# Optimization experiments

Measured on AMD Instinct MI355X. Metric: run time of the kernel, lower is better.

Reference implementation:

```python
import jax, jax.numpy as jnp
import numpy as np

B, S, D, H = 4, 2048, 512, 8
DK = D // H


def setup_inputs() -> dict:
    key = jax.random.key(0)
    ks = jax.random.split(key, 8)
    std = 1.0 / np.sqrt(D)
    return {
        "query": jax.random.normal(ks[0], (B, S, D), jnp.float32),
        "key": jax.random.normal(ks[1], (B, S, D), jnp.float32),
        "value": jax.random.normal(ks[2], (B, S, D), jnp.float32),
        "Wq": jax.random.normal(ks[3], (D, D), jnp.float32) * std,
        "Wk": jax.random.normal(ks[4], (D, D), jnp.float32) * std,
        "Wv": jax.random.normal(ks[5], (D, D), jnp.float32) * std,
        "Wo": jax.random.normal(ks[6], (D, D), jnp.float32) * std,
        "bo": jnp.zeros((D,), jnp.float32),
    }


def reference(query, key, value, Wq, Wk, Wv, Wo, bo):
    # nn.Linear stores weight [out, in]; y = x @ W.T
    def split_heads(x):  # [B,S,D] -> [B,H,S,DK]
        return x.reshape(B, S, H, DK).transpose(0, 2, 1, 3)

    Q = split_heads(query @ Wq.T)
    K = split_heads(key @ Wk.T)
    V = split_heads(value @ Wv.T)
    scale = jnp.sqrt(jnp.asarray(DK, Q.dtype))
    scores = jnp.einsum("bhqd,bhkd->bhqk", Q, K) / scale  # [B,H,S,S]
    attn = jax.nn.softmax(scores, axis=-1)  # dropout=0 / eval mode
    ctx = jnp.einsum("bhqk,bhkd->bhqd", attn, V)
    ctx = ctx.transpose(0, 2, 1, 3).reshape(B, S, D)
    return ctx @ Wo.T + bo
```

## Files before the change

### kernel.cpp

```cpp
#include <hip/hip_runtime.h>
#include <hip/hip_bf16.h>
#include <stdint.h>

#define DEV __device__ __forceinline__

typedef __attribute__((ext_vector_type(8))) __bf16 bf16x8;
typedef __attribute__((ext_vector_type(4))) float f32x4;
typedef __attribute__((ext_vector_type(16))) float f32x16;
typedef __attribute__((ext_vector_type(4))) short short4v;
typedef __attribute__((ext_vector_type(8))) short short8v;
typedef __attribute__((ext_vector_type(4))) unsigned int uint4v;

constexpr int B_ = 4, S_ = 2048, D_ = 512, H_ = 8, DK_ = 64;
constexpr int M_ = B_ * S_;
constexpr int K_ = D_;

DEV unsigned short f2bf(float f) {
  unsigned int u = __builtin_bit_cast(unsigned int, f);
  unsigned int r = (u + 0x7fffu + ((u >> 16) & 1u)) >> 16;
  return (unsigned short)r;
}

DEV void gld16(const void* g, void* l) {
  __builtin_amdgcn_global_load_lds(
      (const __attribute__((address_space(1))) unsigned int*)g,
      (__attribute__((address_space(3))) unsigned int*)l, 16, 0, 0);
}

DEV f32x4 mfma16(bf16x8 a, bf16x8 b, f32x4 c) {
  return __builtin_amdgcn_mfma_f32_16x16x32_bf16(a, b, c, 0, 0, 0);
}
DEV f32x16 mfma32(bf16x8 a, bf16x8 b, f32x16 c) {
  return __builtin_amdgcn_mfma_f32_32x32x16_bf16(a, b, c, 0, 0, 0);
}

DEV short4v tr16(const void* p) {
  short4v d;
  asm volatile("ds_read_b64_tr_b16 %0, %1"
               : "=v"(d)
               : "v"((const __attribute__((address_space(3))) char*)p));
  return d;
}

DEV unsigned pkbf(float a, float b) {
  unsigned r;
  asm("v_cvt_pk_bf16_f32 %0, %1, %2" : "=v"(r) : "v"(a), "v"(b));
  return r;
}

DEV void pl32swap(unsigned& a, unsigned& b) {
  asm volatile("v_permlane32_swap_b32 %0, %1" : "+v"(a), "+v"(b));
}

__global__ __launch_bounds__(256) void convert_all(
    const float* __restrict__ q, const float* __restrict__ k, const float* __restrict__ v,
    const float* __restrict__ wq, const float* __restrict__ wk,
    const float* __restrict__ wv, const float* __restrict__ wo,
    unsigned short* __restrict__ xq, unsigned short* __restrict__ xk,
    unsigned short* __restrict__ xv, unsigned short* __restrict__ wqb,
    unsigned short* __restrict__ wkb, unsigned short* __restrict__ wvb,
    unsigned short* __restrict__ wob)
{
  constexpr int NX = M_ * D_;
  constexpr int NW = D_ * D_;
  constexpr int TOT = (3 * NX + 4 * NW) / 4;
  for (int u = blockIdx.x * blockDim.x + threadIdx.x; u < TOT;
       u += gridDim.x * blockDim.x) {
    int e = u * 4;
    const float* src; unsigned short* dst; int off;
    if (e < 3 * NX) {
      int t = e >> 22; off = e & (NX - 1);
      src = (t == 0) ? q : ((t == 1) ? k : v);
      dst = (t == 0) ? xq : ((t == 1) ? xk : xv);
    } else {
      int e2 = e - 3 * NX;
      int t = e2 >> 18; off = e2 & (NW - 1);
      src = (t == 0) ? wq : ((t == 1) ? wk : ((t == 2) ? wv : wo));
      dst = (t == 0) ? wqb : ((t == 1) ? wkb : ((t == 2) ? wvb : wob));
    }
    float4 f = *(const float4*)(src + off);
    short4v o;
    o.x = (short)f2bf(f.x); o.y = (short)f2bf(f.y);
    o.z = (short)f2bf(f.z); o.w = (short)f2bf(f.w);
    *(short4v*)(dst + off) = o;
  }
}

template <int MODE>
__global__ __launch_bounds__(256, 4) void gemm_bt(
    const unsigned short* __restrict__ A0, const unsigned short* __restrict__ A1,
    const unsigned short* __restrict__ A2,
    const unsigned short* __restrict__ W0, const unsigned short* __restrict__ W1,
    const unsigned short* __restrict__ W2,
    unsigned short* __restrict__ O0, unsigned short* __restrict__ O1,
    unsigned short* __restrict__ O2,
    float* __restrict__ outF, const float* __restrict__ bias)
{
  constexpr int BM = (MODE == 0) ? 128 : 64;
  constexpr int BN = 128, BK = 64, NKT = K_ / BK;
  constexpr int AFR = BM / 32;
  __shared__ unsigned short As[BM * BK];
  __shared__ unsigned short Bs[BN * BK];
  const int tid = threadIdx.x, lane = tid & 63, wave = tid >> 6;
  const int z = blockIdx.z;
  const unsigned short* A = (MODE == 1 || z == 0) ? A0 : (z == 1 ? A1 : A2);
  const unsigned short* W = (MODE == 1 || z == 0) ? W0 : (z == 1 ? W1 : W2);
  unsigned short* outH = (MODE == 1 || z == 0) ? O0 : (z == 1 ? O1 : O2);
  const int bn0 = blockIdx.x * BN, bm0 = blockIdx.y * BM;
  const int wr = (wave >> 1) * (BM / 2), wc = (wave & 1) * 64;
  const int frow = lane & 15, fk16 = (lane >> 4) * 16;

  const char* srcA[AFR];
  int dstA[AFR];
#pragma unroll
  for (int i = 0; i < AFR; ++i) {
    int o = (wave * AFR + i) * 1024;
    int ol = o + lane * 16;
    int row = ol >> 7, off = (ol ^ ((row & 7) << 4)) & 127;
    srcA[i] = (const char*)A + (size_t)(bm0 + row) * (K_ * 2) + off;
    dstA[i] = o;
  }
  const char* srcB[4];
  int dstB[4];
#pragma unroll
  for (int i = 0; i < 4; ++i) {
    int o = (wave * 4 + i) * 1024;
    int ol = o + lane * 16;
    int row = ol >> 7, off = (ol ^ ((row & 7) << 4)) & 127;
    srcB[i] = (const char*)W + (size_t)(bn0 + row) * (K_ * 2) + off;
    dstB[i] = o;
  }

  f32x4 acc[AFR][4];
#pragma unroll
  for (int i = 0; i < AFR; ++i)
#pragma unroll
    for (int j = 0; j < 4; ++j)
#pragma unroll
      for (int r = 0; r < 4; ++r) acc[i][j][r] = 0.f;

  for (int kt = 0; kt < NKT; ++kt) {
    __syncthreads();
#pragma unroll
    for (int i = 0; i < AFR; ++i) gld16(srcA[i] + kt * 128, (char*)As + dstA[i]);
#pragma unroll
    for (int i = 0; i < 4; ++i)   gld16(srcB[i] + kt * 128, (char*)Bs + dstB[i]);
    __syncthreads();
#pragma unroll
    for (int kc = 0; kc < 2; ++kc) {
      bf16x8 a[AFR], b[4];
#pragma unroll
      for (int i = 0; i < AFR; ++i) {
        int row = wr + i * 16 + frow;
        a[i] = *(const bf16x8*)((const char*)As +
                ((row * 128 + kc * 64 + fk16) ^ ((row & 7) << 4)));
      }
#pragma unroll
      for (int j = 0; j < 4; ++j) {
        int row = wc + j * 16 + frow;
        b[j] = *(const bf16x8*)((const char*)Bs +
                ((row * 128 + kc * 64 + fk16) ^ ((row & 7) << 4)));
      }
      __builtin_amdgcn_s_setprio(1);
#pragma unroll
      for (int i = 0; i < AFR; ++i)
#pragma unroll
        for (int j = 0; j < 4; ++j)
          acc[i][j] = mfma16(a[i], b[j], acc[i][j]);
      __builtin_amdgcn_s_setprio(0);
    }
  }

  const int r0 = (lane >> 4) * 4, cn = lane & 15;
  float bv[4];
  if (MODE == 1) {
#pragma unroll
    for (int j = 0; j < 4; ++j) bv[j] = bias[bn0 + wc + j * 16 + cn];
  }
#pragma unroll
  for (int i = 0; i < AFR; ++i)
#pragma unroll
    for (int j = 0; j < 4; ++j)
#pragma unroll
      for (int r = 0; r < 4; ++r) {
        int gm = bm0 + wr + i * 16 + r0 + r;
        int gn = bn0 + wc + j * 16 + cn;
        float val = acc[i][j][r];
        if (MODE == 0) outH[(size_t)gm * D_ + gn] = f2bf(val);
        else           outF[(size_t)gm * D_ + gn] = val + bv[j];
      }
}

__global__ __launch_bounds__(256, 2) void attn(
    const unsigned short* __restrict__ Qm, const unsigned short* __restrict__ Km,
    const unsigned short* __restrict__ Vm, unsigned short* __restrict__ Ctx)
{
  constexpr int QB = 128, KVB = 64, NT = S_ / KVB;
  __shared__ unsigned short Qs[QB * DK_];
  __shared__ unsigned short Kd[2][KVB * DK_];
  __shared__ unsigned short Vd[2][KVB * DK_];
  __shared__ float smA[4][32];
  const int tid = threadIdx.x, lane = tid & 63, wave = tid >> 6;
  const int hi = lane >> 5, l31 = lane & 31, g1 = (lane >> 4) & 1;
  const int bh = blockIdx.y, q0 = blockIdx.x * QB;
  const int bq = bh >> 3, hh = bh & 7;
  const char* Qg = (const char*)(Qm + ((size_t)bq * S_ + q0) * D_ + hh * DK_);
  const char* Kg = (const char*)(Km + (size_t)bq * S_ * D_ + hh * DK_);
  const char* Vg = (const char*)(Vm + (size_t)bq * S_ * D_ + hh * DK_);

  auto stageSwz = [&](const char* gbase, unsigned short* lds, int o) {
    int ol = o + lane * 16;
    int row = ol >> 7, off = (ol ^ ((row & 7) << 4)) & 127;
    gld16(gbase + (size_t)row * 1024 + off, (char*)lds + o);
  };
  auto stageVt = [&](const char* gbase, unsigned short* lds, int o) {
    int ol = o + lane * 16;
    int E0 = ol >> 1;
    int st = E0 >> 6, rr = (E0 >> 4) & 3, c0 = E0 & 15;
    int kk = (st >> 2) * 4 + rr, dd = (st & 3) * 16 + c0;
    gld16(gbase + (size_t)kk * 1024 + dd * 2, (char*)lds + o);
  };

#pragma unroll
  for (int i = 0; i < 4; ++i) stageSwz(Qg, Qs, (wave * 4 + i) * 1024);
#pragma unroll
  for (int i = 0; i < 2; ++i) stageSwz(Kg, Kd[0], (wave * 2 + i) * 1024);
#pragma unroll
  for (int i = 0; i < 2; ++i) stageVt(Vg, Vd[0], (wave * 2 + i) * 1024);
  __syncthreads();

  bf16x8 qf[4];
  {
    int row = wave * 32 + l31;
    int rb = row * 128, sw = (row & 7) << 4;
#pragma unroll
    for (int c = 0; c < 4; ++c)
      qf[c] = *(const bf16x8*)((const char*)Qs + ((rb + c * 32 + hi * 16) ^ sw));
  }

  f32x16 oacc[2];
#pragma unroll
  for (int dt = 0; dt < 2; ++dt)
#pragma unroll
    for (int r = 0; r < 16; ++r) oacc[dt][r] = 0.f;
  float m2 = -1e30f, lsum = 0.f;
  constexpr float SCL2 = 0.125f * 1.44269504089f;

  int cur = 0;
  for (int t = 0; t < NT; ++t) {
    if (t + 1 < NT) {
      const char* Kg1 = Kg + (size_t)(t + 1) * KVB * 1024;
      const char* Vg1 = Vg + (size_t)(t + 1) * KVB * 1024;
#pragma unroll
      for (int i = 0; i < 2; ++i) stageSwz(Kg1, Kd[cur ^ 1], (wave * 2 + i) * 1024);
#pragma unroll
      for (int i = 0; i < 2; ++i) stageVt(Vg1, Vd[cur ^ 1], (wave * 2 + i) * 1024);
    }

    f32x16 sacc[2];
#pragma unroll
    for (int k2 = 0; k2 < 2; ++k2)
#pragma unroll
      for (int r = 0; r < 16; ++r) sacc[k2][r] = 0.f;
    __builtin_amdgcn_s_setprio(1);
#pragma unroll
    for (int c = 0; c < 4; ++c) {
#pragma unroll
      for (int k2 = 0; k2 < 2; ++k2) {
        int row = k2 * 32 + l31;
        bf16x8 kf = *(const bf16x8*)((const char*)Kd[cur] +
                     ((row * 128 + c * 32 + hi * 16) ^ ((row & 7) << 4)));
        sacc[k2] = mfma32(kf, qf[c], sacc[k2]);
      }
    }
    __builtin_amdgcn_s_setprio(0);

    float mloc = sacc[0][0];
#pragma unroll
    for (int k2 = 0; k2 < 2; ++k2)
#pragma unroll
      for (int r = 0; r < 16; ++r) mloc = fmaxf(mloc, sacc[k2][r]);
    mloc = fmaxf(mloc, __shfl_xor(mloc, 32));
    float m2n = fmaxf(m2, mloc * SCL2);
    float alpha = __builtin_amdgcn_exp2f(m2 - m2n);
    m2 = m2n;
    float psum = 0.f;
#pragma unroll
    for (int k2 = 0; k2 < 2; ++k2)
#pragma unroll
      for (int r = 0; r < 16; ++r) {
        float p = __builtin_amdgcn_exp2f(fmaf(sacc[k2][r], SCL2, -m2n));
        sacc[k2][r] = p;
        psum += p;
      }
    psum += __shfl_xor(psum, 32);
    lsum = lsum * alpha + psum;

    if (lane < 32) smA[wave][lane] = alpha;
    f32x4 av[4];
#pragma unroll
    for (int s = 0; s < 4; ++s)
      av[s] = *(const f32x4*)&smA[wave][s * 8 + hi * 4];
#pragma unroll
    for (int dt = 0; dt < 2; ++dt)
#pragma unroll
      for (int r = 0; r < 16; ++r) oacc[dt][r] *= av[r >> 2][r & 3];

    short4v va[4][2][2];
#pragma unroll
    for (int c = 0; c < 4; ++c)
#pragma unroll
      for (int dt = 0; dt < 2; ++dt) {
        int st = 16 * c + 8 * hi + 2 * dt + g1;
        const char* ad = (const char*)Vd[cur] + st * 128 + (lane & 15) * 8;
        va[c][dt][0] = tr16(ad);
        va[c][dt][1] = tr16(ad + 512);
      }
    bf16x8 pfrag[4];
#pragma unroll
    for (int c = 0; c < 4; ++c) {
      const f32x16& P = sacc[c >> 1];
      const int b = (c & 1) * 8;
      unsigned d0 = pkbf(P[b + 0], P[b + 1]);
      unsigned d1 = pkbf(P[b + 2], P[b + 3]);
      unsigned d2 = pkbf(P[b + 4], P[b + 5]);
      unsigned d3 = pkbf(P[b + 6], P[b + 7]);
      pl32swap(d0, d2);
      pl32swap(d1, d3);
      uint4v pi = {d0, d1, d2, d3};
      pfrag[c] = __builtin_bit_cast(bf16x8, pi);
    }
    asm volatile("s_waitcnt lgkmcnt(0)" ::: "memory");
    __builtin_amdgcn_sched_barrier(0);
    __builtin_amdgcn_s_setprio(1);
#pragma unroll
    for (int c = 0; c < 4; ++c)
#pragma unroll
      for (int dt = 0; dt < 2; ++dt) {
        short8v vv = __builtin_shufflevector(va[c][dt][0], va[c][dt][1],
                                             0, 1, 2, 3, 4, 5, 6, 7);
        oacc[dt] = mfma32(pfrag[c], __builtin_bit_cast(bf16x8, vv), oacc[dt]);
      }
    __builtin_amdgcn_s_setprio(0);

    __syncthreads();
    cur ^= 1;
  }

  if (lane < 32) smA[wave][lane] = 1.f / lsum;
  f32x4 iv[4];
#pragma unroll
  for (int s = 0; s < 4; ++s)
    iv[s] = *(const f32x4*)&smA[wave][s * 8 + hi * 4];
#pragma unroll
  for (int dt = 0; dt < 2; ++dt)
#pragma unroll
    for (int r = 0; r < 16; ++r) {
      int qq = (r & 3) + 8 * (r >> 2) + 4 * hi;
      int grow = q0 + wave * 32 + qq;
      int col = hh * 64 + dt * 32 + l31;
      Ctx[((size_t)bq * S_ + grow) * D_ + col] = f2bf(oacc[dt][r] * iv[r >> 2][r & 3]);
    }
}

extern "C" void kernel_launch(void* const* d_in, const int* in_sizes, int n_in,
                              void* d_out, int out_size, void* d_ws, size_t ws_size,
                              hipStream_t stream) {
  const float* q  = (const float*)d_in[0];
  const float* k  = (const float*)d_in[1];
  const float* v  = (const float*)d_in[2];
  const float* wq = (const float*)d_in[3];
  const float* wk = (const float*)d_in[4];
  const float* wv = (const float*)d_in[5];
  const float* wo = (const float*)d_in[6];
  const float* bo = (const float*)d_in[7];
  float* out = (float*)d_out;

  constexpr size_t NX = (size_t)M_ * D_;
  constexpr size_t NW = (size_t)D_ * D_;
  char* ws = (char*)d_ws;
  unsigned short* Xq  = (unsigned short*)ws; ws += NX * 2;
  unsigned short* Xk  = (unsigned short*)ws; ws += NX * 2;
  unsigned short* Xv  = (unsigned short*)ws; ws += NX * 2;
  unsigned short* Wqb = (unsigned short*)ws; ws += NW * 2;
  unsigned short* Wkb = (unsigned short*)ws; ws += NW * 2;
  unsigned short* Wvb = (unsigned short*)ws; ws += NW * 2;
  unsigned short* Wob = (unsigned short*)ws; ws += NW * 2;
  unsigned short* Qbf = (unsigned short*)ws; ws += NX * 2;
  unsigned short* Kbf = (unsigned short*)ws; ws += NX * 2;
  unsigned short* Vbf = (unsigned short*)ws; ws += NX * 2;
  unsigned short* Cx  = (unsigned short*)ws; ws += NX * 2;

  convert_all<<<2048, 256, 0, stream>>>(q, k, v, wq, wk, wv, wo,
                                        Xq, Xk, Xv, Wqb, Wkb, Wvb, Wob);
  gemm_bt<0><<<dim3(4, 64, 3), 256, 0, stream>>>(
      Xq, Xk, Xv, Wqb, Wkb, Wvb, Qbf, Kbf, Vbf, nullptr, nullptr);
  attn<<<dim3(S_ / 128, B_ * H_), 256, 0, stream>>>(Qbf, Kbf, Vbf, Cx);
  gemm_bt<1><<<dim3(4, 128, 1), 256, 0, stream>>>(
      Cx, nullptr, nullptr, Wob, nullptr, nullptr, nullptr, nullptr, nullptr,
      out, bo);
}
```

Measured before the change: 203.1 us.

## Fuse fp32 activation conversion into QKV GEMM and pipeline PV MFMA in attention

The QKV projection GEMM now reads fp32 activations directly and converts them to bf16 in registers before the LDS store, with register prefetch of the next K tile. This drops the separate conversion pass over the three large activation tensors and its round trip through workspace. In attention, the PV MFMA for tile t-1 is deferred into iteration t so it overlaps with the QK scores. The PV product is transposed (V as A operand) so the rescale alpha is per-lane, which removes the LDS broadcast of alpha and 1/lsum and allows packed 8-byte stores of the context. The risks are extra register pressure in both kernels and synchronous global loads for A in the QKV GEMM.

```diff
diff --git a/kernel.cpp b/kernel.cpp
--- a/kernel.cpp
+++ b/kernel.cpp
@@ -10,6 +10,7 @@
 typedef __attribute__((ext_vector_type(4))) short short4v;
 typedef __attribute__((ext_vector_type(8))) short short8v;
 typedef __attribute__((ext_vector_type(4))) unsigned int uint4v;
+typedef __attribute__((ext_vector_type(2))) unsigned int uint2v;
 
 constexpr int B_ = 4, S_ = 2048, D_ = 512, H_ = 8, DK_ = 64;
 constexpr int M_ = B_ * S_;
@@ -52,62 +53,141 @@
   asm volatile("v_permlane32_swap_b32 %0, %1" : "+v"(a), "+v"(b));
 }
 
-__global__ __launch_bounds__(256) void convert_all(
-    const float* __restrict__ q, const float* __restrict__ k, const float* __restrict__ v,
-    const float* __restrict__ wq, const float* __restrict__ wk,
-    const float* __restrict__ wv, const float* __restrict__ wo,
-    unsigned short* __restrict__ xq, unsigned short* __restrict__ xk,
-    unsigned short* __restrict__ xv, unsigned short* __restrict__ wqb,
-    unsigned short* __restrict__ wkb, unsigned short* __restrict__ wvb,
-    unsigned short* __restrict__ wob)
+__global__ __launch_bounds__(256) void convert_w(
+    const float* __restrict__ w0, const float* __restrict__ w1,
+    const float* __restrict__ w2, const float* __restrict__ w3,
+    unsigned short* __restrict__ o0, unsigned short* __restrict__ o1,
+    unsigned short* __restrict__ o2, unsigned short* __restrict__ o3)
 {
-  constexpr int NX = M_ * D_;
-  constexpr int NW = D_ * D_;
-  constexpr int TOT = (3 * NX + 4 * NW) / 4;
-  for (int u = blockIdx.x * blockDim.x + threadIdx.x; u < TOT;
-       u += gridDim.x * blockDim.x) {
-    int e = u * 4;
-    const float* src; unsigned short* dst; int off;
-    if (e < 3 * NX) {
-      int t = e >> 22; off = e & (NX - 1);
-      src = (t == 0) ? q : ((t == 1) ? k : v);
-      dst = (t == 0) ? xq : ((t == 1) ? xk : xv);
-    } else {
-      int e2 = e - 3 * NX;
-      int t = e2 >> 18; off = e2 & (NW - 1);
-      src = (t == 0) ? wq : ((t == 1) ? wk : ((t == 2) ? wv : wo));
-      dst = (t == 0) ? wqb : ((t == 1) ? wkb : ((t == 2) ? wvb : wob));
-    }
-    float4 f = *(const float4*)(src + off);
-    short4v o;
-    o.x = (short)f2bf(f.x); o.y = (short)f2bf(f.y);
-    o.z = (short)f2bf(f.z); o.w = (short)f2bf(f.w);
-    *(short4v*)(dst + off) = o;
-  }
-}
-
-template <int MODE>
-__global__ __launch_bounds__(256, 4) void gemm_bt(
-    const unsigned short* __restrict__ A0, const unsigned short* __restrict__ A1,
-    const unsigned short* __restrict__ A2,
+  int u = blockIdx.x * 256 + threadIdx.x;
+  int t = u >> 16, off = (u & 65535) * 4;
+  const float* src = (t == 0) ? w0 : (t == 1) ? w1 : (t == 2) ? w2 : w3;
+  unsigned short* dst = (t == 0) ? o0 : (t == 1) ? o1 : (t == 2) ? o2 : o3;
+  float4 f = *(const float4*)(src + off);
+  short4v o;
+  o.x = (short)f2bf(f.x); o.y = (short)f2bf(f.y);
+  o.z = (short)f2bf(f.z); o.w = (short)f2bf(f.w);
+  *(short4v*)(dst + off) = o;
+}
+
+__global__ __launch_bounds__(256, 3) void gemm_qkv(
+    const float* __restrict__ A0, const float* __restrict__ A1,
+    const float* __restrict__ A2,
     const unsigned short* __restrict__ W0, const unsigned short* __restrict__ W1,
     const unsigned short* __restrict__ W2,
     unsigned short* __restrict__ O0, unsigned short* __restrict__ O1,
-    unsigned short* __restrict__ O2,
-    float* __restrict__ outF, const float* __restrict__ bias)
+    unsigned short* __restrict__ O2)
 {
-  constexpr int BM = (MODE == 0) ? 128 : 64;
-  constexpr int BN = 128, BK = 64, NKT = K_ / BK;
-  constexpr int AFR = BM / 32;
+  constexpr int BM = 128, BN = 128, BK = 64, NKT = K_ / BK;
   __shared__ unsigned short As[BM * BK];
   __shared__ unsigned short Bs[BN * BK];
   const int tid = threadIdx.x, lane = tid & 63, wave = tid >> 6;
   const int z = blockIdx.z;
-  const unsigned short* A = (MODE == 1 || z == 0) ? A0 : (z == 1 ? A1 : A2);
-  const unsigned short* W = (MODE == 1 || z == 0) ? W0 : (z == 1 ? W1 : W2);
-  unsigned short* outH = (MODE == 1 || z == 0) ? O0 : (z == 1 ? O1 : O2);
+  const float* A = (z == 0) ? A0 : (z == 1 ? A1 : A2);
+  const unsigned short* W = (z == 0) ? W0 : (z == 1 ? W1 : W2);
+  unsigned short* outH = (z == 0) ? O0 : (z == 1 ? O1 : O2);
   const int bn0 = blockIdx.x * BN, bm0 = blockIdx.y * BM;
-  const int wr = (wave >> 1) * (BM / 2), wc = (wave & 1) * 64;
+  const int wr = (wave >> 1) * 64, wc = (wave & 1) * 64;
+  const int frow = lane & 15, fk16 = (lane >> 4) * 16;
+
+  const int srow = tid >> 1, scol = (tid & 1) * 32;
+  const float* asrc = A + (size_t)(bm0 + srow) * K_ + scol;
+  const int abase = srow * 128 + scol * 2, asw = (srow & 7) << 4;
+
+  const char* srcB[4];
+  int dstB[4];
+#pragma unroll
+  for (int i = 0; i < 4; ++i) {
+    int o = (wave * 4 + i) * 1024;
+    int ol = o + lane * 16;
+    int row = ol >> 7, off = (ol ^ ((row & 7) << 4)) & 127;
+    srcB[i] = (const char*)W + (size_t)(bn0 + row) * (K_ * 2) + off;
+    dstB[i] = o;
+  }
+
+  f32x4 acc[4][4];
+#pragma unroll
+  for (int i = 0; i < 4; ++i)
+#pragma unroll
+    for (int j = 0; j < 4; ++j)
+#pragma unroll
+      for (int r = 0; r < 4; ++r) acc[i][j][r] = 0.f;
+
+  float4 xv[8];
+#pragma unroll
+  for (int j = 0; j < 8; ++j) xv[j] = *(const float4*)(asrc + j * 4);
+
+  for (int kt = 0; kt < NKT; ++kt) {
+    __syncthreads();
+    {
+      unsigned dw[16];
+#pragma unroll
+      for (int j = 0; j < 8; ++j) {
+        dw[2 * j]     = pkbf(xv[j].x, xv[j].y);
+        dw[2 * j + 1] = pkbf(xv[j].z, xv[j].w);
+      }
+#pragma unroll
+      for (int c = 0; c < 4; ++c) {
+        uint4v q = {dw[4 * c], dw[4 * c + 1], dw[4 * c + 2], dw[4 * c + 3]};
+        *(uint4v*)((char*)As + ((abase + c * 16) ^ asw)) = q;
+      }
+    }
+#pragma unroll
+    for (int i = 0; i < 4; ++i) gld16(srcB[i] + kt * 128, (char*)Bs + dstB[i]);
+    __syncthreads();
+    if (kt + 1 < NKT) {
+#pragma unroll
+      for (int j = 0; j < 8; ++j)
+        xv[j] = *(const float4*)(asrc + (kt + 1) * 64 + j * 4);
+    }
+#pragma unroll
+    for (int kc = 0; kc < 2; ++kc) {
+      bf16x8 a[4], b[4];
+#pragma unroll
+      for (int i = 0; i < 4; ++i) {
+        int row = wr + i * 16 + frow;
+        a[i] = *(const bf16x8*)((const char*)As +
+                ((row * 128 + kc * 64 + fk16) ^ ((row & 7) << 4)));
+      }
+#pragma unroll
+      for (int j = 0; j < 4; ++j) {
+        int row = wc + j * 16 + frow;
+        b[j] = *(const bf16x8*)((const char*)Bs +
+                ((row * 128 + kc * 64 + fk16) ^ ((row & 7) << 4)));
+      }
+      __builtin_amdgcn_s_setprio(1);
+#pragma unroll
+      for (int i = 0; i < 4; ++i)
+#pragma unroll
+        for (int j = 0; j < 4; ++j)
+          acc[i][j] = mfma16(a[i], b[j], acc[i][j]);
+      __builtin_amdgcn_s_setprio(0);
+    }
+  }
+
+  const int r0 = (lane >> 4) * 4, cn = lane & 15;
+#pragma unroll
+  for (int i = 0; i < 4; ++i)
+#pragma unroll
+    for (int j = 0; j < 4; ++j)
+#pragma unroll
+      for (int r = 0; r < 4; ++r) {
+        int gm = bm0 + wr + i * 16 + r0 + r;
+        int gn = bn0 + wc + j * 16 + cn;
+        outH[(size_t)gm * D_ + gn] = f2bf(acc[i][j][r]);
+      }
+}
+
+__global__ __launch_bounds__(256, 4) void gemm_out(
+    const unsigned short* __restrict__ A, const unsigned short* __restrict__ W,
+    float* __restrict__ outF, const float* __restrict__ bias)
+{
+  constexpr int BM = 64, BN = 128, BK = 64, NKT = K_ / BK, AFR = 2;
+  __shared__ unsigned short As[BM * BK];
+  __shared__ unsigned short Bs[BN * BK];
+  const int tid = threadIdx.x, lane = tid & 63, wave = tid >> 6;
+  const int bn0 = blockIdx.x * BN, bm0 = blockIdx.y * BM;
+  const int wr = (wave >> 1) * 32, wc = (wave & 1) * 64;
   const int frow = lane & 15, fk16 = (lane >> 4) * 16;
 
   const char* srcA[AFR];
@@ -173,10 +253,8 @@
 
   const int r0 = (lane >> 4) * 4, cn = lane & 15;
   float bv[4];
-  if (MODE == 1) {
-#pragma unroll
-    for (int j = 0; j < 4; ++j) bv[j] = bias[bn0 + wc + j * 16 + cn];
-  }
+#pragma unroll
+  for (int j = 0; j < 4; ++j) bv[j] = bias[bn0 + wc + j * 16 + cn];
 #pragma unroll
   for (int i = 0; i < AFR; ++i)
 #pragma unroll
@@ -185,9 +263,7 @@
       for (int r = 0; r < 4; ++r) {
         int gm = bm0 + wr + i * 16 + r0 + r;
         int gn = bn0 + wc + j * 16 + cn;
-        float val = acc[i][j][r];
-        if (MODE == 0) outH[(size_t)gm * D_ + gn] = f2bf(val);
-        else           outF[(size_t)gm * D_ + gn] = val + bv[j];
+        outF[(size_t)gm * D_ + gn] = acc[i][j][r] + bv[j];
       }
 }
 
@@ -199,7 +275,6 @@
   __shared__ unsigned short Qs[QB * DK_];
   __shared__ unsigned short Kd[2][KVB * DK_];
   __shared__ unsigned short Vd[2][KVB * DK_];
-  __shared__ float smA[4][32];
   const int tid = threadIdx.x, lane = tid & 63, wave = tid >> 6;
   const int hi = lane >> 5, l31 = lane & 31, g1 = (lane >> 4) & 1;
   const int bh = blockIdx.y, q0 = blockIdx.x * QB;
@@ -246,6 +321,19 @@
   float m2 = -1e30f, lsum = 0.f;
   constexpr float SCL2 = 0.125f * 1.44269504089f;
 
+  short4v va[4][2][2];
+  bf16x8 pfrag[4];
+#pragma unroll
+  for (int c = 0; c < 4; ++c) {
+#pragma unroll
+    for (int dt = 0; dt < 2; ++dt) {
+      va[c][dt][0] = short4v{0, 0, 0, 0};
+      va[c][dt][1] = short4v{0, 0, 0, 0};
+    }
+    uint4v zz = {0u, 0u, 0u, 0u};
+    pfrag[c] = __builtin_bit_cast(bf16x8, zz);
+  }
+
   int cur = 0;
   for (int t = 0; t < NT; ++t) {
     if (t + 1 < NT) {
@@ -273,6 +361,14 @@
         sacc[k2] = mfma32(kf, qf[c], sacc[k2]);
       }
     }
+#pragma unroll
+    for (int c = 0; c < 4; ++c)
+#pragma unroll
+      for (int dt = 0; dt < 2; ++dt) {
+        short8v vv = __builtin_shufflevector(va[c][dt][0], va[c][dt][1],
+                                             0, 1, 2, 3, 4, 5, 6, 7);
+        oacc[dt] = mfma32(__builtin_bit_cast(bf16x8, vv), pfrag[c], oacc[dt]);
+      }
     __builtin_amdgcn_s_setprio(0);
 
     float mloc = sacc[0][0];
@@ -296,17 +392,11 @@
     psum += __shfl_xor(psum, 32);
     lsum = lsum * alpha + psum;
 
-    if (lane < 32) smA[wave][lane] = alpha;
-    f32x4 av[4];
-#pragma unroll
-    for (int s = 0; s < 4; ++s)
-      av[s] = *(const f32x4*)&smA[wave][s * 8 + hi * 4];
 #pragma unroll
     for (int dt = 0; dt < 2; ++dt)
 #pragma unroll
-      for (int r = 0; r < 16; ++r) oacc[dt][r] *= av[r >> 2][r & 3];
-
-    short4v va[4][2][2];
+      for (int r = 0; r < 16; ++r) oacc[dt][r] *= alpha;
+
 #pragma unroll
     for (int c = 0; c < 4; ++c)
 #pragma unroll
@@ -316,7 +406,6 @@
         va[c][dt][0] = tr16(ad);
         va[c][dt][1] = tr16(ad + 512);
       }
-    bf16x8 pfrag[4];
 #pragma unroll
     for (int c = 0; c < 4; ++c) {
       const f32x16& P = sacc[c >> 1];
@@ -330,36 +419,33 @@
       uint4v pi = {d0, d1, d2, d3};
       pfrag[c] = __builtin_bit_cast(bf16x8, pi);
     }
-    asm volatile("s_waitcnt lgkmcnt(0)" ::: "memory");
-    __builtin_amdgcn_sched_barrier(0);
-    __builtin_amdgcn_s_setprio(1);
-#pragma unroll
-    for (int c = 0; c < 4; ++c)
-#pragma unroll
-      for (int dt = 0; dt < 2; ++dt) {
-        short8v vv = __builtin_shufflevector(va[c][dt][0], va[c][dt][1],
-                                             0, 1, 2, 3, 4, 5, 6, 7);
-        oacc[dt] = mfma32(pfrag[c], __builtin_bit_cast(bf16x8, vv), oacc[dt]);
-      }
-    __builtin_amdgcn_s_setprio(0);
 
     __syncthreads();
     cur ^= 1;
   }
 
-  if (lane < 32) smA[wave][lane] = 1.f / lsum;
-  f32x4 iv[4];
-#pragma unroll
-  for (int s = 0; s < 4; ++s)
-    iv[s] = *(const f32x4*)&smA[wave][s * 8 + hi * 4];
+  __builtin_amdgcn_s_setprio(1);
+#pragma unroll
+  for (int c = 0; c < 4; ++c)
+#pragma unroll
+    for (int dt = 0; dt < 2; ++dt) {
+      short8v vv = __builtin_shufflevector(va[c][dt][0], va[c][dt][1],
+                                           0, 1, 2, 3, 4, 5, 6, 7);
+      oacc[dt] = mfma32(__builtin_bit_cast(bf16x8, vv), pfrag[c], oacc[dt]);
+    }
+  __builtin_amdgcn_s_setprio(0);
+
+  const float inv = 1.f / lsum;
+  unsigned short* crow =
+      Ctx + ((size_t)bq * S_ + q0 + wave * 32 + l31) * D_ + hh * DK_;
 #pragma unroll
   for (int dt = 0; dt < 2; ++dt)
 #pragma unroll
-    for (int r = 0; r < 16; ++r) {
-      int qq = (r & 3) + 8 * (r >> 2) + 4 * hi;
-      int grow = q0 + wave * 32 + qq;
-      int col = hh * 64 + dt * 32 + l31;
-      Ctx[((size_t)bq * S_ + grow) * D_ + col] = f2bf(oacc[dt][r] * iv[r >> 2][r & 3]);
+    for (int g = 0; g < 4; ++g) {
+      uint2v pk;
+      pk.x = pkbf(oacc[dt][4 * g + 0] * inv, oacc[dt][4 * g + 1] * inv);
+      pk.y = pkbf(oacc[dt][4 * g + 2] * inv, oacc[dt][4 * g + 3] * inv);
+      *(uint2v*)(crow + dt * 32 + 8 * g + 4 * hi) = pk;
     }
 }
 
@@ -379,9 +465,6 @@
   constexpr size_t NX = (size_t)M_ * D_;
   constexpr size_t NW = (size_t)D_ * D_;
   char* ws = (char*)d_ws;
-  unsigned short* Xq  = (unsigned short*)ws; ws += NX * 2;
-  unsigned short* Xk  = (unsigned short*)ws; ws += NX * 2;
-  unsigned short* Xv  = (unsigned short*)ws; ws += NX * 2;
   unsigned short* Wqb = (unsigned short*)ws; ws += NW * 2;
   unsigned short* Wkb = (unsigned short*)ws; ws += NW * 2;
   unsigned short* Wvb = (unsigned short*)ws; ws += NW * 2;
@@ -391,12 +474,9 @@
   unsigned short* Vbf = (unsigned short*)ws; ws += NX * 2;
   unsigned short* Cx  = (unsigned short*)ws; ws += NX * 2;
 
-  convert_all<<<2048, 256, 0, stream>>>(q, k, v, wq, wk, wv, wo,
-                                        Xq, Xk, Xv, Wqb, Wkb, Wvb, Wob);
-  gemm_bt<0><<<dim3(4, 64, 3), 256, 0, stream>>>(
-      Xq, Xk, Xv, Wqb, Wkb, Wvb, Qbf, Kbf, Vbf, nullptr, nullptr);
+  convert_w<<<1024, 256, 0, stream>>>(wq, wk, wv, wo, Wqb, Wkb, Wvb, Wob);
+  gemm_qkv<<<dim3(4, 64, 3), 256, 0, stream>>>(
+      q, k, v, Wqb, Wkb, Wvb, Qbf, Kbf, Vbf);
   attn<<<dim3(S_ / 128, B_ * H_), 256, 0, stream>>>(Qbf, Kbf, Vbf, Cx);
-  gemm_bt<1><<<dim3(4, 128, 1), 256, 0, stream>>>(
-      Cx, nullptr, nullptr, Wob, nullptr, nullptr, nullptr, nullptr, nullptr,
-      out, bo);
-}
+  gemm_out<<<dim3(4, 128), 256, 0, stream>>>(Cx, Wob, out, bo);
+}
```

After: 201.0 us. No clear change (-1.1%).
